# Performance work log

Measured on AMD Instinct MI355X. Metric: run time of the kernel, lower is better.

## Reference

```python
import jax, jax.numpy as jnp
import numpy as np

B, S, D, H = 4, 2048, 1024, 16
DK = D // H


def setup_inputs() -> dict:
    key = jax.random.key(0)
    ks = jax.random.split(key, 11)
    s = 1.0 / np.sqrt(D)
    return {
        "x_Q": jax.random.normal(ks[0], (B, S, D), jnp.float32),
        "x_K": jax.random.normal(ks[1], (B, S, D), jnp.float32),
        "x_V": jax.random.normal(ks[2], (B, S, D), jnp.float32),
        "Wq": jax.random.normal(ks[3], (D, D), jnp.float32) * s,
        "bq": jax.random.normal(ks[4], (D,), jnp.float32) * 0.01,
        "Wk": jax.random.normal(ks[5], (D, D), jnp.float32) * s,
        "bk": jax.random.normal(ks[6], (D,), jnp.float32) * 0.01,
        "Wv": jax.random.normal(ks[7], (D, D), jnp.float32) * s,
        "bv": jax.random.normal(ks[8], (D,), jnp.float32) * 0.01,
        "Wo": jax.random.normal(ks[9], (D, D), jnp.float32) * s,
        "bo": jax.random.normal(ks[10], (D,), jnp.float32) * 0.01,
    }


def reference(x_Q, x_K, x_V, Wq, bq, Wk, bk, Wv, bv, Wo, bo):
    def heads(x, W, b):
        # [B,S,D] -> [B,H,S,DK]
        y = x @ W.T + b
        return y.reshape(B, S, H, DK).transpose(0, 2, 1, 3)

    Q = heads(x_Q, Wq, bq)
    K = heads(x_K, Wk, bk)
    V = heads(x_V, Wv, bv)
    scores = jnp.einsum('bhqd,bhkd->bhqk', Q, K) / jnp.sqrt(jnp.float32(DK))
    probs = jax.nn.softmax(scores, axis=-1)
    out = jnp.einsum('bhqk,bhkd->bhqd', probs, V)
    out = out.transpose(0, 2, 1, 3).reshape(B, S, D)
    return out @ Wo.T + bo
```

## Files before the change

kernel.cpp:

```cpp
#include <hip/hip_runtime.h>

typedef __attribute__((ext_vector_type(8))) short bf16x8;
typedef __attribute__((ext_vector_type(4))) short short4v;
typedef __attribute__((ext_vector_type(4))) float f32x4;
typedef __attribute__((ext_vector_type(16))) float f32x16;
typedef __attribute__((ext_vector_type(2))) unsigned int u32x2;

#define DEV static __device__ __forceinline__

#define QSC 0.1804165017087941f

DEV unsigned short f2b(float f) {
  union { float f; unsigned int i; } v; v.f = f;
  unsigned int x = v.i;
  return (unsigned short)((x + 0x7FFFu + ((x >> 16) & 1u)) >> 16);
}

DEV void cp16(const unsigned short* g, unsigned short* l) {
  __builtin_amdgcn_global_load_lds(
      (const __attribute__((address_space(1))) void*)g,
      (__attribute__((address_space(3))) void*)l, 16, 0, 0);
}

DEV unsigned int cvtpk(float lo, float hi) {
  unsigned int r;
  asm("v_cvt_pk_bf16_f32 %0, %1, %2" : "=v"(r) : "v"(lo), "v"(hi));
  return r;
}

__global__ void cvt_kernel(const float* __restrict__ in,
                           unsigned short* __restrict__ out, int n, float scale) {
  const int i = (blockIdx.x * blockDim.x + threadIdx.x) * 4;
  if (i < n) {
    const float4 v = *(const float4*)&in[i];
    short4v o;
    o[0] = (short)f2b(v.x * scale); o[1] = (short)f2b(v.y * scale);
    o[2] = (short)f2b(v.z * scale); o[3] = (short)f2b(v.w * scale);
    *(short4v*)&out[i] = o;
  }
}

__global__ void cvt_all(const float* __restrict__ xq, const float* __restrict__ xk,
                        const float* __restrict__ xv, const float* __restrict__ wq,
                        const float* __restrict__ wk, const float* __restrict__ wv,
                        const float* __restrict__ wo, unsigned short* __restrict__ X,
                        unsigned short* __restrict__ W) {
  const int b = blockIdx.x;
  const float* p;
  unsigned short* out;
  float scale = 1.f;
  int i;
  if (b < 24576) {
    const int seg = b >> 13, ib = b & 8191;
    p = (seg == 0) ? xq : (seg == 1) ? xk : xv;
    out = X + (size_t)seg * 8388608;
    i = (ib * 256 + threadIdx.x) * 4;
  } else {
    const int bb = b - 24576;
    const int seg = bb >> 10, ib = bb & 1023;
    p = (seg == 0) ? wq : (seg == 1) ? wk : (seg == 2) ? wv : wo;
    out = W + (size_t)seg * 1048576;
    if (seg == 0) scale = QSC;
    i = (ib * 256 + threadIdx.x) * 4;
  }
  const float4 v = *(const float4*)&p[i];
  short4v o;
  o[0] = (short)f2b(v.x * scale); o[1] = (short)f2b(v.y * scale);
  o[2] = (short)f2b(v.z * scale); o[3] = (short)f2b(v.w * scale);
  *(short4v*)&out[i] = o;
}

template <int MODE>
DEV void gemm_tile_body(const unsigned short* __restrict__ A,
                        const unsigned short* __restrict__ W,
                        const float* __restrict__ bias, void* __restrict__ OutV,
                        unsigned short* sA, unsigned short* sB,
                        int bm, int bn, int N, int K, float bsc) {
  const int tid = threadIdx.x;
  const int lane = tid & 63, wave = tid >> 6;
  const int lr = lane & 15, quad = lane >> 4;
  const int wm = (wave >> 1) * 64, wn = (wave & 1) * 64;
  const int srow = tid >> 3;
  const int sdst = (tid & 7) * 8;
  const int ssrc = ((tid & 7) ^ (srow & 7)) * 8;

  f32x4 acc[4][4] = {};

  for (int kt = 0; kt < K; kt += 64) {
#pragma unroll
    for (int is = 0; is < 4; ++is) {
      const int r = is * 32 + srow;
      cp16(&A[(size_t)(bm + r) * K + kt + ssrc], &sA[r * 64 + sdst]);
      cp16(&W[(size_t)(bn + r) * K + kt + ssrc], &sB[r * 64 + sdst]);
    }
    __syncthreads();
#pragma unroll
    for (int ks = 0; ks < 2; ++ks) {
      bf16x8 af[4], bf[4];
      const int co = (((ks * 4 + quad) ^ (lr & 7)) << 3);
#pragma unroll
      for (int i = 0; i < 4; ++i)
        af[i] = *(const bf16x8*)&sA[(wm + i * 16 + lr) * 64 + co];
#pragma unroll
      for (int j = 0; j < 4; ++j)
        bf[j] = *(const bf16x8*)&sB[(wn + j * 16 + lr) * 64 + co];
#pragma unroll
      for (int i = 0; i < 4; ++i)
#pragma unroll
        for (int j = 0; j < 4; ++j)
          acc[i][j] = __builtin_amdgcn_mfma_f32_16x16x32_bf16(af[i], bf[j], acc[i][j], 0, 0, 0);
    }
    __syncthreads();
  }

#pragma unroll
  for (int j = 0; j < 4; ++j) {
    const int n = bn + wn + j * 16 + lr;
    const float bv = bias[n] * bsc;
#pragma unroll
    for (int i = 0; i < 4; ++i) {
      const int mb = bm + wm + i * 16 + quad * 4;
      if (MODE == 2) {
        u32x2 w;
        w[0] = cvtpk(acc[i][j][0] + bv, acc[i][j][1] + bv);
        w[1] = cvtpk(acc[i][j][2] + bv, acc[i][j][3] + bv);
        *(u32x2*)&((unsigned short*)OutV)[
            ((size_t)((mb >> 11) * 16 + (n >> 6)) * 64 + (n & 63)) * 2048 + (mb & 2047)] = w;
      } else {
#pragma unroll
        for (int r = 0; r < 4; ++r) {
          const int m = mb + r;
          const float o = acc[i][j][r] + bv;
          if (MODE == 0) {
            ((float*)OutV)[(size_t)m * N + n] = o;
          } else {
            ((unsigned short*)OutV)[((size_t)((m >> 11) * 16 + (n >> 6)) * 2048 + (m & 2047)) * 64 + (n & 63)] = f2b(o);
          }
        }
      }
    }
  }
}

template <int MODE>
__global__ __launch_bounds__(256, 3) void gemm_bt(
    const unsigned short* __restrict__ A, const unsigned short* __restrict__ W,
    const float* __restrict__ bias, void* __restrict__ OutV,
    int N, int K, float bsc) {
  __shared__ __align__(16) unsigned short sA[128 * 64];
  __shared__ __align__(16) unsigned short sB[128 * 64];
  const int wg = blockIdx.x + (blockIdx.y << 6);
  const int xcd = wg & 7;
  const int j = wg >> 3;
  const int bn = (j & 7) * 128;
  const int bm = (xcd * 8 + (j >> 3)) * 128;
  gemm_tile_body<MODE>(A, W, bias, OutV, sA, sB, bm, bn, N, K, bsc);
}

__global__ __launch_bounds__(256, 3) void gemm_qkv3(
    const unsigned short* __restrict__ Aall, const unsigned short* __restrict__ Wall,
    const float* __restrict__ b0, const float* __restrict__ b1,
    const float* __restrict__ b2, unsigned short* __restrict__ Out) {
  __shared__ __align__(16) unsigned short sA[128 * 64];
  __shared__ __align__(16) unsigned short sB[128 * 64];
  const int wg = blockIdx.x + (blockIdx.y << 6) + (blockIdx.z << 9);
  const int xcd = wg & 7;
  const int j = wg >> 3;
  const int bn = (j & 7) * 128;
  const int g = xcd * 24 + (j >> 3);
  const int z = g >> 6;
  const int bm = (g & 63) * 128;
  const unsigned short* A = Aall + (size_t)z * 8388608;
  const unsigned short* W = Wall + (size_t)z * 1048576;
  const float* bias = (z == 0) ? b0 : (z == 1) ? b1 : b2;
  const float bsc = (z == 0) ? QSC : 1.f;
  void* OutV = (void*)(Out + (size_t)z * 8388608);
  if (z == 2)
    gemm_tile_body<2>(A, W, bias, OutV, sA, sB, bm, bn, 1024, 1024, bsc);
  else
    gemm_tile_body<1>(A, W, bias, OutV, sA, sB, bm, bn, 1024, 1024, bsc);
}

#define ATTN_PACK8(SREG, RB, KD)                                               \
  {                                                                            \
    float pr[8];                                                               \
    _Pragma("unroll") for (int r = 0; r < 8; ++r) {                            \
      pr[r] = __builtin_amdgcn_exp2f(SREG[(RB) + r]);                          \
      rsp[r & 3] += pr[r];                                                     \
    }                                                                          \
    const u32x2 w02 = __builtin_amdgcn_permlane32_swap(                        \
        cvtpk(pr[0], pr[1]), cvtpk(pr[4], pr[5]), false, false);               \
    const u32x2 w13 = __builtin_amdgcn_permlane32_swap(                        \
        cvtpk(pr[2], pr[3]), cvtpk(pr[6], pr[7]), false, false);               \
    pa[KD].w[0] = w02[0]; pa[KD].w[1] = w13[0];                                \
    pa[KD].w[2] = w02[1]; pa[KD].w[3] = w13[1];                                \
  }

#define ATTN_TILE(T, SKB, SVB, DKB, DVB)                                       \
  {                                                                            \
    if ((T) + 1 < 32) {                                                        \
      const int kvn = ((T) + 1) * 64;                                          \
      _Pragma("unroll") for (int is = 0; is < 2; ++is) {                       \
        const int r = is * 32 + sr_;                                           \
        const int sw = (sc_ ^ ((r ^ (r >> 3)) & 7)) * 8;                       \
        cp16(&Kp[(size_t)(kvn + r) * 64 + sw], &DKB[r * 64 + sc_ * 8]);        \
        cp16(&Vp[(size_t)r * 2048 + kvn + sw], &DVB[r * 64 + sc_ * 8]);        \
      }                                                                        \
    }                                                                          \
    {                                                                          \
      f32x16 s0 = {};                                                          \
      __builtin_amdgcn_s_setprio(1);                                           \
      _Pragma("unroll") for (int ks = 0; ks < 4; ++ks) {                       \
        const bf16x8 k0 = *(const bf16x8*)&SKB[rowa + (((ks * 2 + b5) ^ swa) << 3)]; \
        s0 = __builtin_amdgcn_mfma_f32_32x32x16_bf16(k0, qf[ks], s0, 0, 0, 0); \
      }                                                                        \
      __builtin_amdgcn_s_setprio(0);                                           \
      ATTN_PACK8(s0, 0, 0)                                                     \
      ATTN_PACK8(s0, 8, 1)                                                     \
    }                                                                          \
    __builtin_amdgcn_s_setprio(1);                                             \
    _Pragma("unroll") for (int ks = 0; ks < 2; ++ks) {                         \
      const bf16x8 va = *(const bf16x8*)&SVB[rowa + (((ks * 2 + b5) ^ swa) << 3)]; \
      const bf16x8 vb = *(const bf16x8*)&SVB[rowb + (((ks * 2 + b5) ^ swb) << 3)]; \
      oacc0 = __builtin_amdgcn_mfma_f32_32x32x16_bf16(pa[ks].v, va, oacc0, 0, 0, 0); \
      oacc1 = __builtin_amdgcn_mfma_f32_32x32x16_bf16(pa[ks].v, vb, oacc1, 0, 0, 0); \
    }                                                                          \
    __builtin_amdgcn_s_setprio(0);                                             \
    {                                                                          \
      f32x16 s1 = {};                                                          \
      __builtin_amdgcn_s_setprio(1);                                           \
      _Pragma("unroll") for (int ks = 0; ks < 4; ++ks) {                       \
        const bf16x8 k1 = *(const bf16x8*)&SKB[rowb + (((ks * 2 + b5) ^ swb) << 3)]; \
        s1 = __builtin_amdgcn_mfma_f32_32x32x16_bf16(k1, qf[ks], s1, 0, 0, 0); \
      }                                                                        \
      __builtin_amdgcn_s_setprio(0);                                           \
      ATTN_PACK8(s1, 0, 0)                                                     \
      ATTN_PACK8(s1, 8, 1)                                                     \
    }                                                                          \
    __builtin_amdgcn_s_setprio(1);                                             \
    _Pragma("unroll") for (int ks = 2; ks < 4; ++ks) {                         \
      const bf16x8 va = *(const bf16x8*)&SVB[rowa + (((ks * 2 + b5) ^ swa) << 3)]; \
      const bf16x8 vb = *(const bf16x8*)&SVB[rowb + (((ks * 2 + b5) ^ swb) << 3)]; \
      oacc0 = __builtin_amdgcn_mfma_f32_32x32x16_bf16(pa[ks - 2].v, va, oacc0, 0, 0, 0); \
      oacc1 = __builtin_amdgcn_mfma_f32_32x32x16_bf16(pa[ks - 2].v, vb, oacc1, 0, 0, 0); \
    }                                                                          \
    __builtin_amdgcn_s_setprio(0);                                             \
    __syncthreads();                                                           \
  }

__global__ __launch_bounds__(256, 3) void attn_kernel(
    const unsigned short* __restrict__ Qb, const unsigned short* __restrict__ Kb,
    const unsigned short* __restrict__ Vt, unsigned short* __restrict__ Ob) {
  __shared__ __align__(16) unsigned short sK[2][64 * 64];
  __shared__ __align__(16) unsigned short sV[2][64 * 64];

  const int tid = threadIdx.x;
  const int lane = tid & 63;
  const int wave = tid >> 6;
  const int c31 = lane & 31;
  const int b5 = lane >> 5;

  const int wg = blockIdx.y * 16 + blockIdx.x;
  const int j = wg >> 3;
  const int bh = (wg & 7) * 8 + (j >> 4);
  const int q0 = (j & 15) * 128 + wave * 32;

  const size_t base = (size_t)bh * (2048 * 64);
  const unsigned short* __restrict__ Qp = Qb + base;
  const unsigned short* __restrict__ Kp = Kb + base;
  const unsigned short* __restrict__ Vp = Vt + base;

  bf16x8 qf[4];
#pragma unroll
  for (int ks = 0; ks < 4; ++ks)
    qf[ks] = *(const bf16x8*)&Qp[(size_t)(q0 + c31) * 64 + ks * 16 + b5 * 8];

  f32x16 oacc0 = {}, oacc1 = {};
  float rsp[4] = {0.f, 0.f, 0.f, 0.f};
  union PA { unsigned int w[4]; bf16x8 v; };
  PA pa[2];

  const int sr_ = tid >> 3;
  const int sc_ = tid & 7;

  const int swa = (c31 ^ (c31 >> 3)) & 7;
  const int swb = swa ^ 4;
  const int rowa = c31 * 64, rowb = (32 + c31) * 64;

  unsigned short* sK0 = &sK[0][0];
  unsigned short* sK1 = &sK[1][0];
  unsigned short* sV0 = &sV[0][0];
  unsigned short* sV1 = &sV[1][0];

#pragma unroll
  for (int is = 0; is < 2; ++is) {
    const int r = is * 32 + sr_;
    const int sw = (sc_ ^ ((r ^ (r >> 3)) & 7)) * 8;
    cp16(&Kp[(size_t)r * 64 + sw], &sK0[r * 64 + sc_ * 8]);
    cp16(&Vp[(size_t)r * 2048 + sw], &sV0[r * 64 + sc_ * 8]);
  }
  __syncthreads();

  for (int t = 0; t < 32; t += 2) {
    ATTN_TILE(t, sK0, sV0, sK1, sV1);
    ATTN_TILE(t + 1, sK1, sV1, sK0, sV0);
  }

  float rs = (rsp[0] + rsp[1]) + (rsp[2] + rsp[3]);
  rs += __shfl_xor(rs, 32);
  const float linv = 1.f / rs;
  const int b = bh >> 4, h = bh & 15;
#pragma unroll
  for (int r = 0; r < 16; ++r) {
    const int crow = (r & 3) + 8 * (r >> 2) + 4 * b5;
    const float li = __shfl(linv, crow);
    unsigned short* op = &Ob[(size_t)(b * 2048 + q0 + crow) * 1024 + h * 64];
    op[c31] = f2b(oacc0[r] * li);
    op[32 + c31] = f2b(oacc1[r] * li);
  }
}

extern "C" void kernel_launch(void* const* d_in, const int* in_sizes, int n_in,
                              void* d_out, int out_size, void* d_ws, size_t ws_size,
                              hipStream_t stream) {
  const float* xq = (const float*)d_in[0];
  const float* xk = (const float*)d_in[1];
  const float* xv = (const float*)d_in[2];
  const float* Wq = (const float*)d_in[3];
  const float* bq = (const float*)d_in[4];
  const float* Wk = (const float*)d_in[5];
  const float* bk = (const float*)d_in[6];
  const float* Wv = (const float*)d_in[7];
  const float* bv = (const float*)d_in[8];
  const float* Wo = (const float*)d_in[9];
  const float* bo = (const float*)d_in[10];

  unsigned short* ws = (unsigned short*)d_ws;
  const size_t SZ = (size_t)8192 * 1024;
  const size_t WSZ = (size_t)1024 * 1024;

  if (ws_size >= (6 * SZ + 4 * WSZ) * sizeof(unsigned short)) {
    unsigned short* Xall = ws;
    unsigned short* Wall = ws + 3 * SZ;
    unsigned short* Qb = Wall + 4 * WSZ;
    unsigned short* Kb = Qb + SZ;
    unsigned short* Vt = Kb + SZ;

    hipLaunchKernelGGL(cvt_all, dim3(28672), dim3(256), 0, stream,
                       xq, xk, xv, Wq, Wk, Wv, Wo, Xall, Wall);
    hipLaunchKernelGGL(gemm_qkv3, dim3(64, 8, 3), dim3(256), 0, stream,
                       Xall, Wall, bq, bk, bv, Qb);
    hipLaunchKernelGGL(attn_kernel, dim3(16, 64), dim3(256), 0, stream, Qb, Kb, Vt, Xall);
    hipLaunchKernelGGL((gemm_bt<0>), dim3(64, 8), dim3(256), 0, stream,
                       Xall, Wall + 3 * WSZ, bo, d_out, 1024, 1024, 1.f);
  } else {
    unsigned short* X  = ws;
    unsigned short* Wb = ws + SZ;
    unsigned short* Qb = ws + SZ + SZ / 8;
    unsigned short* Kb = Qb + SZ;
    unsigned short* Vt = Kb + SZ;

    const int NX = 8192 * 1024, NW = 1024 * 1024;
    dim3 cbx(256), cgx(NX / 1024), cgw(NW / 1024);
    dim3 gg(64, 8), bb(256);

    hipLaunchKernelGGL(cvt_kernel, cgx, cbx, 0, stream, xq, X, NX, 1.f);
    hipLaunchKernelGGL(cvt_kernel, cgw, cbx, 0, stream, Wq, Wb, NW, QSC);
    hipLaunchKernelGGL((gemm_bt<1>), gg, bb, 0, stream, X, Wb, bq, (void*)Qb, 1024, 1024, QSC);

    hipLaunchKernelGGL(cvt_kernel, cgx, cbx, 0, stream, xk, X, NX, 1.f);
    hipLaunchKernelGGL(cvt_kernel, cgw, cbx, 0, stream, Wk, Wb, NW, 1.f);
    hipLaunchKernelGGL((gemm_bt<1>), gg, bb, 0, stream, X, Wb, bk, (void*)Kb, 1024, 1024, 1.f);

    hipLaunchKernelGGL(cvt_kernel, cgx, cbx, 0, stream, xv, X, NX, 1.f);
    hipLaunchKernelGGL(cvt_kernel, cgw, cbx, 0, stream, Wv, Wb, NW, 1.f);
    hipLaunchKernelGGL((gemm_bt<2>), gg, bb, 0, stream, X, Wb, bv, (void*)Vt, 1024, 1024, 1.f);

    hipLaunchKernelGGL(attn_kernel, dim3(16, 64), bb, 0, stream, Qb, Kb, Vt, X);

    hipLaunchKernelGGL(cvt_kernel, cgw, cbx, 0, stream, Wo, Wb, NW, 1.f);
    hipLaunchKernelGGL((gemm_bt<0>), gg, bb, 0, stream, X, Wb, bo, d_out, 1024, 1024, 1.f);
  }
}
```

Baseline: 333.8 us.

## Replace 128x128 projection GEMMs with double-buffered 256x256-tile GEMM kernels

Adds a 512-thread GEMM body with 256x256 output tiles in which each wave computes a 128x64 sub-tile, and uses it for both the fused QKV projection and the output projection. The body double-buffers LDS, prefetching the next K-slab via global_load_lds while the current one feeds the MFMAs, and raises priority around the MFMA loop. The goal is more operand reuse per LDS load and overlap of global loads with compute. In exchange, each block uses about 128 KB of LDS, and the grids shrink to 384 and 128 blocks. That risks poor CU occupancy and tail imbalance, especially for the output GEMM.

```diff
diff --git a/kernel.cpp b/kernel.cpp
--- a/kernel.cpp
+++ b/kernel.cpp
@@ -70,6 +70,140 @@
   *(short4v*)&out[i] = o;
 }
 
+#define G256_STAGE(KT, DA, DB)                                                 \
+  _Pragma("unroll") for (int is = 0; is < 4; ++is) {                           \
+    const int r = is * 64 + srow;                                              \
+    cp16(&A[(size_t)(bm + r) * K + (KT) + ssrc], &DA[r * 64 + sdst]);          \
+    cp16(&W[(size_t)(bn + r) * K + (KT) + ssrc], &DB[r * 64 + sdst]);          \
+  }
+
+template <int MODE>
+DEV void gemm256_body(const unsigned short* __restrict__ A,
+                      const unsigned short* __restrict__ W,
+                      const float* __restrict__ bias, void* __restrict__ OutV,
+                      unsigned short* sA0, unsigned short* sA1,
+                      unsigned short* sB0, unsigned short* sB1,
+                      int bm, int bn, int N, int K, float bsc) {
+  const int tid = threadIdx.x;
+  const int lane = tid & 63, wid = tid >> 6;
+  const int lr = lane & 15, quad = lane >> 4;
+  const int wm = (wid >> 2) * 128;
+  const int wn = (wid & 3) * 64;
+  const int srow = tid >> 3;
+  const int sdst = (tid & 7) * 8;
+  const int ssrc = ((tid & 7) ^ (srow & 7)) * 8;
+
+  f32x4 acc[8][4] = {};
+
+  unsigned short *cA = sA0, *cB = sB0, *nA = sA1, *nB = sB1;
+  const int nk = K >> 6;
+
+  G256_STAGE(0, cA, cB);
+
+  for (int t = 0; t < nk; ++t) {
+    if (t + 1 < nk) {
+      G256_STAGE((t + 1) << 6, nA, nB);
+      asm volatile("s_waitcnt vmcnt(8)" ::: "memory");
+    } else {
+      asm volatile("s_waitcnt vmcnt(0)" ::: "memory");
+    }
+    __builtin_amdgcn_s_barrier();
+    __builtin_amdgcn_sched_barrier(0);
+
+#pragma unroll
+    for (int ks = 0; ks < 2; ++ks) {
+      bf16x8 af[8], bf[4];
+      const int co = (((ks * 4 + quad) ^ (lr & 7)) << 3);
+#pragma unroll
+      for (int i = 0; i < 8; ++i)
+        af[i] = *(const bf16x8*)&cA[(wm + i * 16 + lr) * 64 + co];
+#pragma unroll
+      for (int j = 0; j < 4; ++j)
+        bf[j] = *(const bf16x8*)&cB[(wn + j * 16 + lr) * 64 + co];
+      __builtin_amdgcn_s_setprio(1);
+#pragma unroll
+      for (int i = 0; i < 8; ++i)
+#pragma unroll
+        for (int j = 0; j < 4; ++j)
+          acc[i][j] = __builtin_amdgcn_mfma_f32_16x16x32_bf16(af[i], bf[j], acc[i][j], 0, 0, 0);
+      __builtin_amdgcn_s_setprio(0);
+    }
+
+    __builtin_amdgcn_s_barrier();
+    __builtin_amdgcn_sched_barrier(0);
+    unsigned short* tA = cA; cA = nA; nA = tA;
+    unsigned short* tB = cB; cB = nB; nB = tB;
+  }
+
+#pragma unroll
+  for (int j = 0; j < 4; ++j) {
+    const int n = bn + wn + j * 16 + lr;
+    const float bv = bias[n] * bsc;
+#pragma unroll
+    for (int i = 0; i < 8; ++i) {
+      const int mb = bm + wm + i * 16 + quad * 4;
+      if (MODE == 2) {
+        u32x2 w;
+        w[0] = cvtpk(acc[i][j][0] + bv, acc[i][j][1] + bv);
+        w[1] = cvtpk(acc[i][j][2] + bv, acc[i][j][3] + bv);
+        *(u32x2*)&((unsigned short*)OutV)[
+            ((size_t)((mb >> 11) * 16 + (n >> 6)) * 64 + (n & 63)) * 2048 + (mb & 2047)] = w;
+      } else {
+#pragma unroll
+        for (int r = 0; r < 4; ++r) {
+          const int m = mb + r;
+          const float o = acc[i][j][r] + bv;
+          if (MODE == 0) {
+            ((float*)OutV)[(size_t)m * N + n] = o;
+          } else {
+            ((unsigned short*)OutV)[((size_t)((m >> 11) * 16 + (n >> 6)) * 2048 + (m & 2047)) * 64 + (n & 63)] = f2b(o);
+          }
+        }
+      }
+    }
+  }
+}
+
+__global__ __launch_bounds__(512, 2) void gemm256_out(
+    const unsigned short* __restrict__ A, const unsigned short* __restrict__ W,
+    const float* __restrict__ bias, void* __restrict__ OutV, int N, int K) {
+  __shared__ __align__(16) unsigned short sA[2][256 * 64];
+  __shared__ __align__(16) unsigned short sB[2][256 * 64];
+  const int wg = blockIdx.x + (blockIdx.y << 5);
+  const int xcd = wg & 7;
+  const int j = wg >> 3;
+  const int bn = (j & 3) * 256;
+  const int bm = (xcd * 4 + (j >> 2)) * 256;
+  gemm256_body<0>(A, W, bias, OutV, &sA[0][0], &sA[1][0], &sB[0][0], &sB[1][0],
+                  bm, bn, N, K, 1.f);
+}
+
+__global__ __launch_bounds__(512, 2) void gemm256_qkv(
+    const unsigned short* __restrict__ Aall, const unsigned short* __restrict__ Wall,
+    const float* __restrict__ b0, const float* __restrict__ b1,
+    const float* __restrict__ b2, unsigned short* __restrict__ Out) {
+  __shared__ __align__(16) unsigned short sA[2][256 * 64];
+  __shared__ __align__(16) unsigned short sB[2][256 * 64];
+  const int wg = blockIdx.x + (blockIdx.y << 5) + (blockIdx.z << 7);
+  const int xcd = wg & 7;
+  const int j = wg >> 3;
+  const int bn = (j & 3) * 256;
+  const int g = xcd * 12 + (j >> 2);
+  const int z = g >> 5;
+  const int bm = (g & 31) * 256;
+  const unsigned short* A = Aall + (size_t)z * 8388608;
+  const unsigned short* W = Wall + (size_t)z * 1048576;
+  const float* bias = (z == 0) ? b0 : (z == 1) ? b1 : b2;
+  const float bsc = (z == 0) ? QSC : 1.f;
+  void* OutV = (void*)(Out + (size_t)z * 8388608);
+  if (z == 2)
+    gemm256_body<2>(A, W, bias, OutV, &sA[0][0], &sA[1][0], &sB[0][0], &sB[1][0],
+                    bm, bn, 1024, 1024, bsc);
+  else
+    gemm256_body<1>(A, W, bias, OutV, &sA[0][0], &sA[1][0], &sB[0][0], &sB[1][0],
+                    bm, bn, 1024, 1024, bsc);
+}
+
 template <int MODE>
 DEV void gemm_tile_body(const unsigned short* __restrict__ A,
                         const unsigned short* __restrict__ W,
@@ -155,30 +289,6 @@
   const int bn = (j & 7) * 128;
   const int bm = (xcd * 8 + (j >> 3)) * 128;
   gemm_tile_body<MODE>(A, W, bias, OutV, sA, sB, bm, bn, N, K, bsc);
-}
-
-__global__ __launch_bounds__(256, 3) void gemm_qkv3(
-    const unsigned short* __restrict__ Aall, const unsigned short* __restrict__ Wall,
-    const float* __restrict__ b0, const float* __restrict__ b1,
-    const float* __restrict__ b2, unsigned short* __restrict__ Out) {
-  __shared__ __align__(16) unsigned short sA[128 * 64];
-  __shared__ __align__(16) unsigned short sB[128 * 64];
-  const int wg = blockIdx.x + (blockIdx.y << 6) + (blockIdx.z << 9);
-  const int xcd = wg & 7;
-  const int j = wg >> 3;
-  const int bn = (j & 7) * 128;
-  const int g = xcd * 24 + (j >> 3);
-  const int z = g >> 6;
-  const int bm = (g & 63) * 128;
-  const unsigned short* A = Aall + (size_t)z * 8388608;
-  const unsigned short* W = Wall + (size_t)z * 1048576;
-  const float* bias = (z == 0) ? b0 : (z == 1) ? b1 : b2;
-  const float bsc = (z == 0) ? QSC : 1.f;
-  void* OutV = (void*)(Out + (size_t)z * 8388608);
-  if (z == 2)
-    gemm_tile_body<2>(A, W, bias, OutV, sA, sB, bm, bn, 1024, 1024, bsc);
-  else
-    gemm_tile_body<1>(A, W, bias, OutV, sA, sB, bm, bn, 1024, 1024, bsc);
 }
 
 #define ATTN_PACK8(SREG, RB, KD)                                               \
@@ -348,11 +458,11 @@
 
     hipLaunchKernelGGL(cvt_all, dim3(28672), dim3(256), 0, stream,
                        xq, xk, xv, Wq, Wk, Wv, Wo, Xall, Wall);
-    hipLaunchKernelGGL(gemm_qkv3, dim3(64, 8, 3), dim3(256), 0, stream,
+    hipLaunchKernelGGL(gemm256_qkv, dim3(32, 4, 3), dim3(512), 0, stream,
                        Xall, Wall, bq, bk, bv, Qb);
     hipLaunchKernelGGL(attn_kernel, dim3(16, 64), dim3(256), 0, stream, Qb, Kb, Vt, Xall);
-    hipLaunchKernelGGL((gemm_bt<0>), dim3(64, 8), dim3(256), 0, stream,
-                       Xall, Wall + 3 * WSZ, bo, d_out, 1024, 1024, 1.f);
+    hipLaunchKernelGGL(gemm256_out, dim3(32, 4), dim3(512), 0, stream,
+                       Xall, Wall + 3 * WSZ, bo, d_out, 1024, 1024);
   } else {
     unsigned short* X  = ws;
     unsigned short* Wb = ws + SZ;
```

After: 348.6 us. 4.4% more time.
